# Kernel optimization log

Hardware: AMD Instinct MI355X
Metric: run time of the kernel (lower is better)

Reference implementation:

```python
import jax, jax.numpy as jnp
import numpy as np
import math

D = 2048
NH = 16
HD = D // NH
MULT = 4
EPS = 1e-6


def rmsnorm(x, g):
    norm = jax.lax.rsqrt(jnp.mean(x * x, axis=-1, keepdims=True) + EPS)
    return g * x * norm


def setup_inputs() -> dict:
    key = jax.random.key(0)
    ks = jax.random.split(key, 8)
    s = 0.02  # keep activations in a sane range
    return {
        "x": jax.random.normal(ks[0], (2, 2048, D), dtype=jnp.float32),
        "g1": jnp.ones((D,), dtype=jnp.float32),
        "wq": jax.random.normal(ks[1], (D, D), dtype=jnp.float32) * s,
        "wk": jax.random.normal(ks[2], (D, D), dtype=jnp.float32) * s,
        "wv": jax.random.normal(ks[3], (D, D), dtype=jnp.float32) * s,
        "wo": jax.random.normal(ks[4], (D, D), dtype=jnp.float32) * s,
        "g2": jnp.ones((D,), dtype=jnp.float32),
        "w_up": jax.random.normal(ks[5], (2 * D * MULT, D), dtype=jnp.float32) * s,
        "w_down": jax.random.normal(ks[6], (D, D * MULT), dtype=jnp.float32) * s,
    }


def reference(x, g1, wq, wk, wv, wo, g2, w_up, w_down):
    B, T, _ = x.shape
    # --- causal self-attention with pre-RMSNorm ---
    h = rmsnorm(x, g1)
    q = (h @ wq.T).reshape(B, T, NH, HD).transpose(0, 2, 1, 3)  # [B,H,T,hd]
    k = (h @ wk.T).reshape(B, T, NH, HD).transpose(0, 2, 1, 3)
    v = (h @ wv.T).reshape(B, T, NH, HD).transpose(0, 2, 1, 3)
    att = jnp.einsum("bhtd,bhsd->bhts", q, k) / math.sqrt(HD)  # [B,H,T,T]
    neg = jnp.finfo(att.dtype).min
    causal = jnp.triu(jnp.full((T, T), neg, dtype=att.dtype), k=1)
    att = att + causal
    w = jax.nn.softmax(att, axis=-1)
    z = jnp.einsum("bhts,bhsd->bhtd", w, v)  # [B,H,T,hd]
    z = z.transpose(0, 2, 1, 3).reshape(B, T, D)
    x = x + z @ wo.T
    # --- SwiGLU-style FFN (GELU gate) with pre-RMSNorm ---
    h2 = rmsnorm(x, g2)
    uv = h2 @ w_up.T  # [B,T,2*D*MULT]
    u, vgate = jnp.split(uv, 2, axis=-1)
    ff = (jax.nn.gelu(u, approximate=False) * vgate) @ w_down.T
    return x + ff
```

## Files before the change

kernel.cpp:

```cpp
#include <hip/hip_runtime.h>
#include <math.h>

typedef __bf16 bf16_t;
typedef __bf16 bf16x8 __attribute__((ext_vector_type(8)));
typedef __bf16 bf16x4 __attribute__((ext_vector_type(4)));
typedef float f32x4 __attribute__((ext_vector_type(4)));

#define D_MODEL 2048
#define N_HEADS 16
#define HEAD_D 128
#define SEQ 2048
#define NTOK 4096
#define DFF 8192
#define UPN 16384

#define GLDS16(g, l) __builtin_amdgcn_global_load_lds( \
    (const __attribute__((address_space(1))) void*)(g), \
    (__attribute__((address_space(3))) void*)(l), 16, 0, 0)

#define MFMA16(a, b, c) __builtin_amdgcn_mfma_f32_16x16x32_bf16((a), (b), (c), 0, 0, 0)

__global__ __launch_bounds__(256) void cvt_bf16_kernel(const float* __restrict__ in,
                                                       bf16_t* __restrict__ out, long n4) {
    long i = (long)blockIdx.x * 256 + threadIdx.x;
    long stride = (long)gridDim.x * 256;
    for (; i < n4; i += stride) {
        float4 f = ((const float4*)in)[i];
        bf16x4 v;
        v[0] = (bf16_t)f.x; v[1] = (bf16_t)f.y; v[2] = (bf16_t)f.z; v[3] = (bf16_t)f.w;
        ((bf16x4*)out)[i] = v;
    }
}

__global__ __launch_bounds__(256) void rmsnorm_kernel(const float* __restrict__ x,
                                                      const float* __restrict__ g,
                                                      bf16_t* __restrict__ out) {
    int row = blockIdx.x;
    const float* xr = x + (size_t)row * D_MODEL;
    int c0 = threadIdx.x * 8;
    float4 a = *(const float4*)&xr[c0];
    float4 b = *(const float4*)&xr[c0 + 4];
    float ss = a.x*a.x + a.y*a.y + a.z*a.z + a.w*a.w
             + b.x*b.x + b.y*b.y + b.z*b.z + b.w*b.w;
    #pragma unroll
    for (int off = 1; off < 64; off <<= 1) ss += __shfl_xor(ss, off);
    __shared__ float red[4];
    if ((threadIdx.x & 63) == 0) red[threadIdx.x >> 6] = ss;
    __syncthreads();
    float norm = rsqrtf((red[0] + red[1] + red[2] + red[3]) * (1.f / D_MODEL) + 1e-6f);
    float4 ga = *(const float4*)&g[c0];
    float4 gb = *(const float4*)&g[c0 + 4];
    bf16x8 o;
    o[0] = (bf16_t)(a.x * ga.x * norm); o[1] = (bf16_t)(a.y * ga.y * norm);
    o[2] = (bf16_t)(a.z * ga.z * norm); o[3] = (bf16_t)(a.w * ga.w * norm);
    o[4] = (bf16_t)(b.x * gb.x * norm); o[5] = (bf16_t)(b.y * gb.y * norm);
    o[6] = (bf16_t)(b.z * gb.z * norm); o[7] = (bf16_t)(b.w * gb.w * norm);
    *(bf16x8*)&out[(size_t)row * D_MODEL + c0] = o;
}

__global__ __launch_bounds__(256) void combine3_kernel(const float* __restrict__ r,
        const float* __restrict__ p0, const float* __restrict__ p1,
        float* __restrict__ out, long n4) {
    long i = (long)blockIdx.x * 256 + threadIdx.x;
    long stride = (long)gridDim.x * 256;
    for (; i < n4; i += stride) {
        float4 a = ((const float4*)r)[i];
        float4 b = ((const float4*)p0)[i];
        float4 c = ((const float4*)p1)[i];
        float4 o; o.x = a.x+b.x+c.x; o.y = a.y+b.y+c.y; o.z = a.z+b.z+c.z; o.w = a.w+b.w+c.w;
        ((float4*)out)[i] = o;
    }
}

template<int MODE, int KSPLIT>
__global__ __launch_bounds__(512, 2)
void gemm256(const bf16_t* __restrict__ A, const bf16_t* __restrict__ W,
             void* __restrict__ o0, void* __restrict__ o1, void* __restrict__ o2,
             const float* __restrict__ res, int nbx, int K)
{
    __shared__ __align__(16) bf16_t ldsA[2 * 2 * 8192];
    __shared__ __align__(16) bf16_t ldsB[2 * 2 * 8192];
    const int tid = threadIdx.x;
    const int wave = tid >> 6, lane = tid & 63;
    const int lr = lane & 15, lg = lane >> 4;
    const int wm = wave >> 2, wn = wave & 3;

    const int nwg = gridDim.x, bid = blockIdx.x;
    const int cpx = nwg >> 3;
    const int s = (bid & 7) * cpx + (bid >> 3);
    const int by = s & 15, bx = s >> 4;
    const int bm0 = by * 256;
    const int bn0 = (MODE == 2) ? bx * 128 : bx * 256;
    const int z = (KSPLIT == 2) ? blockIdx.z : 0;
    const int Keff = K / KSPLIT, koff = z * Keff;

    const int rl = wave * 16 + (lane >> 2);
    const int gsw = ((lane & 3) ^ ((rl >> 1) & 3)) * 8;
    const bf16_t* asrc = A + (size_t)(bm0 + rl) * K + koff + gsw;
    const bf16_t* bsrc;
    size_t bstep2;
    if constexpr (MODE == 2) {
        int grp = rl >> 6, wi = rl & 63;
        int brow = (wi < 32) ? (bn0 + grp * 32 + wi) : (DFF + bn0 + grp * 32 + (wi - 32));
        bsrc = W + (size_t)brow * K + koff + gsw;
        bstep2 = (size_t)64 * K;
    } else {
        bsrc = W + (size_t)(bn0 + rl) * K + koff + gsw;
        bstep2 = (size_t)128 * K;
    }

    auto stA = [&](int t, int kh) {
        char* d = (char*)ldsA + (((t & 1) * 2 + kh) * 16384) + wave * 1024 + lane * 16;
        const bf16_t* sp = asrc + (size_t)t * 64 + kh * 32;
        GLDS16(sp, d);
        GLDS16(sp + (size_t)128 * K, d + 8192);
    };
    auto stB = [&](int t, int kh) {
        char* d = (char*)ldsB + (((t & 1) * 2 + kh) * 16384) + wave * 1024 + lane * 16;
        const bf16_t* sp = bsrc + (size_t)t * 64 + kh * 32;
        GLDS16(sp, d);
        GLDS16(sp + bstep2, d + 8192);
    };

    f32x4 acc[8][4] = {};
    const int xg = (lg ^ ((lr >> 1) & 3)) * 8;
    const int NKT = Keff >> 6;

    stA(0, 0); stA(0, 1); stB(0, 0); stB(0, 1); stA(1, 0);
    asm volatile("s_waitcnt vmcnt(2)" ::: "memory");
    __builtin_amdgcn_s_barrier();
    __builtin_amdgcn_sched_barrier(0);

    for (int t = 0; t < NKT; ++t) {
        const bf16_t* Ab = ldsA + ((t & 1) * 2) * 8192;
        const bf16_t* Bb = ldsB + ((t & 1) * 2) * 8192;
        const bool s1 = (t + 1 < NKT), s2 = (t + 2 < NKT);
        bf16x8 af[4], bfr[4];

        #pragma unroll
        for (int i = 0; i < 4; ++i)
            af[i] = *(const bf16x8*)&Ab[(wm * 128 + i * 16 + lr) * 32 + xg];
        #pragma unroll
        for (int n = 0; n < 4; ++n)
            bfr[n] = *(const bf16x8*)&Bb[(wn * 64 + n * 16 + lr) * 32 + xg];
        if (s1) { stA(t + 1, 1); stB(t + 1, 0); }
        __builtin_amdgcn_s_barrier();
        __builtin_amdgcn_sched_barrier(0);
        __builtin_amdgcn_s_setprio(1);
        #pragma unroll
        for (int i = 0; i < 4; ++i)
            #pragma unroll
            for (int n = 0; n < 4; ++n)
                acc[i][n] = MFMA16(af[i], bfr[n], acc[i][n]);
        __builtin_amdgcn_s_setprio(0);
        __builtin_amdgcn_s_barrier();
        __builtin_amdgcn_sched_barrier(0);

        #pragma unroll
        for (int i = 0; i < 4; ++i)
            af[i] = *(const bf16x8*)&Ab[(wm * 128 + (i + 4) * 16 + lr) * 32 + xg];
        if (s1) stB(t + 1, 1);
        __builtin_amdgcn_s_barrier();
        __builtin_amdgcn_sched_barrier(0);
        __builtin_amdgcn_s_setprio(1);
        #pragma unroll
        for (int i = 0; i < 4; ++i)
            #pragma unroll
            for (int n = 0; n < 4; ++n)
                acc[i + 4][n] = MFMA16(af[i], bfr[n], acc[i + 4][n]);
        __builtin_amdgcn_s_setprio(0);
        __builtin_amdgcn_s_barrier();
        __builtin_amdgcn_sched_barrier(0);

        #pragma unroll
        for (int i = 0; i < 4; ++i)
            af[i] = *(const bf16x8*)&Ab[8192 + (wm * 128 + i * 16 + lr) * 32 + xg];
        #pragma unroll
        for (int n = 0; n < 4; ++n)
            bfr[n] = *(const bf16x8*)&Bb[8192 + (wn * 64 + n * 16 + lr) * 32 + xg];
        __builtin_amdgcn_s_barrier();
        __builtin_amdgcn_sched_barrier(0);
        __builtin_amdgcn_s_setprio(1);
        #pragma unroll
        for (int i = 0; i < 4; ++i)
            #pragma unroll
            for (int n = 0; n < 4; ++n)
                acc[i][n] = MFMA16(af[i], bfr[n], acc[i][n]);
        __builtin_amdgcn_s_setprio(0);
        __builtin_amdgcn_s_barrier();
        __builtin_amdgcn_sched_barrier(0);

        #pragma unroll
        for (int i = 0; i < 4; ++i)
            af[i] = *(const bf16x8*)&Ab[8192 + (wm * 128 + (i + 4) * 16 + lr) * 32 + xg];
        if (s2) {
            stA(t + 2, 0);
            asm volatile("s_waitcnt vmcnt(2)" ::: "memory");
        } else {
            asm volatile("s_waitcnt vmcnt(0)" ::: "memory");
        }
        __builtin_amdgcn_s_barrier();
        __builtin_amdgcn_sched_barrier(0);
        __builtin_amdgcn_s_setprio(1);
        #pragma unroll
        for (int i = 0; i < 4; ++i)
            #pragma unroll
            for (int n = 0; n < 4; ++n)
                acc[i + 4][n] = MFMA16(af[i], bfr[n], acc[i + 4][n]);
        __builtin_amdgcn_s_setprio(0);
        __builtin_amdgcn_s_barrier();
        __builtin_amdgcn_sched_barrier(0);
    }

    if constexpr (MODE == 0) {
        const float qs = 0.08838834764831845f;
        const int th = bn0 >> 11;
        #pragma unroll
        for (int m = 0; m < 8; ++m) {
            int grow = bm0 + wm * 128 + m * 16 + lg * 4;
            #pragma unroll
            for (int n = 0; n < 4; ++n) {
                int gcol = bn0 + wn * 64 + n * 16 + lr;
                int c = gcol & 2047;
                if (th == 0) {
                    #pragma unroll
                    for (int r = 0; r < 4; ++r)
                        ((bf16_t*)o0)[(size_t)(grow + r) * D_MODEL + c] = (bf16_t)(acc[m][n][r] * qs);
                } else if (th == 1) {
                    #pragma unroll
                    for (int r = 0; r < 4; ++r)
                        ((bf16_t*)o1)[(size_t)(grow + r) * D_MODEL + c] = (bf16_t)acc[m][n][r];
                } else {
                    int hh = c >> 7, d = c & 127;
                    int bb = grow >> 11, t0 = grow & 2047;
                    bf16x4 st;
                    #pragma unroll
                    for (int r = 0; r < 4; ++r) st[r] = (bf16_t)acc[m][n][r];
                    *(bf16x4*)&((bf16_t*)o2)[((size_t)(bb * N_HEADS + hh) * HEAD_D + d) * SEQ + t0] = st;
                }
            }
        }
    } else if constexpr (MODE == 1) {
        float* po = (KSPLIT == 2) ? ((float*)o0 + (size_t)z * NTOK * D_MODEL) : (float*)o0;
        #pragma unroll
        for (int m = 0; m < 8; ++m) {
            int grow = bm0 + wm * 128 + m * 16 + lg * 4;
            #pragma unroll
            for (int n = 0; n < 4; ++n) {
                int gcol = bn0 + wn * 64 + n * 16 + lr;
                #pragma unroll
                for (int r = 0; r < 4; ++r) {
                    size_t idx = (size_t)(grow + r) * D_MODEL + gcol;
                    if (KSPLIT == 2) po[idx] = acc[m][n][r];
                    else             po[idx] = res[idx] + acc[m][n][r];
                }
            }
        }
    } else {
        #pragma unroll
        for (int m = 0; m < 8; ++m) {
            int grow = bm0 + wm * 128 + m * 16 + lg * 4;
            #pragma unroll
            for (int n = 0; n < 2; ++n) {
                int gcol = bn0 + wn * 32 + n * 16 + lr;
                #pragma unroll
                for (int r = 0; r < 4; ++r) {
                    float u = acc[m][n][r], vg = acc[m][n + 2][r];
                    float ge = 0.5f * u * (1.f + erff(u * 0.70710678118654752f));
                    ((bf16_t*)o0)[(size_t)(grow + r) * DFF + gcol] = (bf16_t)(ge * vg);
                }
            }
        }
    }
}

__global__ __launch_bounds__(256)
void attn_kernel(const bf16_t* __restrict__ Q, const bf16_t* __restrict__ K,
                 const bf16_t* __restrict__ Vt, bf16_t* __restrict__ Z)
{
    const int qt = gridDim.x - 1 - blockIdx.x;
    const int h = blockIdx.y, b = blockIdx.z;
    const int q0 = qt * 64;
    const int tid = threadIdx.x, wave = tid >> 6, lane = tid & 63;
    const int lr = lane & 15, lg = lane >> 4;

    __shared__ __align__(16) bf16_t Qs[64 * 136];
    __shared__ __align__(16) bf16_t Ks[64 * 136];
    __shared__ __align__(16) bf16_t Vts[128 * 72];
    __shared__ __align__(16) bf16_t Ps[4][16 * 72];

    const size_t base = ((size_t)b * SEQ) * D_MODEL + (size_t)h * HEAD_D;
    const size_t vbase = (size_t)(b * N_HEADS + h) * HEAD_D * SEQ;

    #pragma unroll
    for (int i = 0; i < 4; ++i) {
        int v = tid + 256 * i;
        int row = v >> 4, cv = (v & 15) * 8;
        *(uint4*)&Qs[row * 136 + cv] = *(const uint4*)&Q[base + (size_t)(q0 + row) * D_MODEL + cv];
    }

    f32x4 o[8] = {};
    float mrun[4], lrun[4];
    #pragma unroll
    for (int r = 0; r < 4; ++r) { mrun[r] = -1e30f; lrun[r] = 0.f; }

    for (int kt = 0; kt <= qt; ++kt) {
        const int k0 = kt * 64;
        __syncthreads();
        #pragma unroll
        for (int i = 0; i < 4; ++i) {
            int v = tid + 256 * i;
            int row = v >> 4, cv = (v & 15) * 8;
            *(uint4*)&Ks[row * 136 + cv] = *(const uint4*)&K[base + (size_t)(k0 + row) * D_MODEL + cv];
            int d = v >> 3, c8 = (v & 7) * 8;
            *(uint4*)&Vts[d * 72 + c8] = *(const uint4*)&Vt[vbase + (size_t)d * SEQ + k0 + c8];
        }
        __syncthreads();

        f32x4 sv[4] = {};
        #pragma unroll
        for (int kk = 0; kk < 4; ++kk) {
            bf16x8 aq = *(const bf16x8*)&Qs[(wave * 16 + lr) * 136 + kk * 32 + lg * 8];
            #pragma unroll
            for (int nb = 0; nb < 4; ++nb) {
                bf16x8 bk = *(const bf16x8*)&Ks[(nb * 16 + lr) * 136 + kk * 32 + lg * 8];
                sv[nb] = MFMA16(aq, bk, sv[nb]);
            }
        }
        if (kt == qt) {
            #pragma unroll
            for (int nb = 0; nb < 4; ++nb)
                #pragma unroll
                for (int r = 0; r < 4; ++r) {
                    int qrel = 16 * wave + lg * 4 + r;
                    int krel = nb * 16 + lr;
                    if (krel > qrel) sv[nb][r] = -1e30f;
                }
        }
        float resc[4];
        #pragma unroll
        for (int r = 0; r < 4; ++r) {
            float mx = fmaxf(fmaxf(sv[0][r], sv[1][r]), fmaxf(sv[2][r], sv[3][r]));
            #pragma unroll
            for (int off = 1; off < 16; off <<= 1) mx = fmaxf(mx, __shfl_xor(mx, off));
            float mnew = fmaxf(mrun[r], mx);
            resc[r] = __expf(mrun[r] - mnew);
            float sum = 0.f;
            #pragma unroll
            for (int nb = 0; nb < 4; ++nb) {
                float p = __expf(sv[nb][r] - mnew);
                sv[nb][r] = p;
                sum += p;
            }
            #pragma unroll
            for (int off = 1; off < 16; off <<= 1) sum += __shfl_xor(sum, off);
            lrun[r] = lrun[r] * resc[r] + sum;
            mrun[r] = mnew;
        }
        #pragma unroll
        for (int ob = 0; ob < 8; ++ob)
            #pragma unroll
            for (int r = 0; r < 4; ++r) o[ob][r] *= resc[r];
        #pragma unroll
        for (int nb = 0; nb < 4; ++nb)
            #pragma unroll
            for (int r = 0; r < 4; ++r)
                Ps[wave][(lg * 4 + r) * 72 + nb * 16 + lr] = (bf16_t)sv[nb][r];
        #pragma unroll
        for (int kk = 0; kk < 2; ++kk) {
            bf16x8 ap = *(const bf16x8*)&Ps[wave][lr * 72 + kk * 32 + lg * 8];
            #pragma unroll
            for (int ob = 0; ob < 8; ++ob) {
                bf16x8 bv = *(const bf16x8*)&Vts[(ob * 16 + lr) * 72 + kk * 32 + lg * 8];
                o[ob] = MFMA16(ap, bv, o[ob]);
            }
        }
    }
    #pragma unroll
    for (int ob = 0; ob < 8; ++ob)
        #pragma unroll
        for (int r = 0; r < 4; ++r) {
            int t = q0 + 16 * wave + lg * 4 + r;
            Z[base + (size_t)t * D_MODEL + ob * 16 + lr] = (bf16_t)(o[ob][r] / lrun[r]);
        }
}

extern "C" void kernel_launch(void* const* d_in, const int* in_sizes, int n_in,
                              void* d_out, int out_size, void* d_ws, size_t ws_size,
                              hipStream_t stream)
{
    const float* x   = (const float*)d_in[0];
    const float* g1  = (const float*)d_in[1];
    const float* wq  = (const float*)d_in[2];
    const float* wk  = (const float*)d_in[3];
    const float* wv  = (const float*)d_in[4];
    const float* wo  = (const float*)d_in[5];
    const float* g2  = (const float*)d_in[6];
    const float* wup = (const float*)d_in[7];
    const float* wdn = (const float*)d_in[8];
    float* out = (float*)d_out;

    char* wsp = (char*)d_ws;
    size_t off = 0;
    auto alloc = [&](size_t bytes) { void* p = wsp + off; off += (bytes + 255) & ~255ull; return p; };
    bf16_t* wq_b  = (bf16_t*)alloc((size_t)D_MODEL * D_MODEL * 2);
    bf16_t* wk_b  = (bf16_t*)alloc((size_t)D_MODEL * D_MODEL * 2);
    bf16_t* wv_b  = (bf16_t*)alloc((size_t)D_MODEL * D_MODEL * 2);
    bf16_t* wo_b  = (bf16_t*)alloc((size_t)D_MODEL * D_MODEL * 2);
    bf16_t* wup_b = (bf16_t*)alloc((size_t)UPN * D_MODEL * 2);
    bf16_t* wdn_b = (bf16_t*)alloc((size_t)D_MODEL * DFF * 2);
    bf16_t* h_b   = (bf16_t*)alloc((size_t)NTOK * D_MODEL * 2);
    bf16_t* q_b   = (bf16_t*)alloc((size_t)NTOK * D_MODEL * 2);
    bf16_t* k_b   = (bf16_t*)alloc((size_t)NTOK * D_MODEL * 2);
    bf16_t* vt_b  = (bf16_t*)alloc((size_t)NTOK * D_MODEL * 2);
    bf16_t* z_b   = (bf16_t*)alloc((size_t)NTOK * D_MODEL * 2);
    float*  x1    = (float*) alloc((size_t)NTOK * D_MODEL * 4);
    bf16_t* h2_b  = (bf16_t*)alloc((size_t)NTOK * D_MODEL * 2);
    bf16_t* act_b = (bf16_t*)alloc((size_t)NTOK * DFF * 2);
    float* pbuf = (float*)h_b;

    auto cvt = [&](const float* in, bf16_t* outb, long n) {
        long n4 = n / 4;
        long nb = (n4 + 255) / 256;
        int blocks = nb > 2048 ? 2048 : (int)nb;
        cvt_bf16_kernel<<<blocks, 256, 0, stream>>>(in, outb, n4);
    };
    cvt(wq,  wq_b,  (long)D_MODEL * D_MODEL);
    cvt(wk,  wk_b,  (long)D_MODEL * D_MODEL);
    cvt(wv,  wv_b,  (long)D_MODEL * D_MODEL);
    cvt(wo,  wo_b,  (long)D_MODEL * D_MODEL);
    cvt(wup, wup_b, (long)UPN * D_MODEL);
    cvt(wdn, wdn_b, (long)D_MODEL * DFF);

    rmsnorm_kernel<<<NTOK, 256, 0, stream>>>(x, g1, h_b);

    gemm256<0, 1><<<24 * 16, 512, 0, stream>>>(h_b, wq_b, q_b, k_b, vt_b, nullptr, 24, D_MODEL);

    attn_kernel<<<dim3(SEQ / 64, N_HEADS, 2), 256, 0, stream>>>(q_b, k_b, vt_b, z_b);

    gemm256<1, 2><<<dim3(8 * 16, 1, 2), 512, 0, stream>>>(z_b, wo_b, pbuf, nullptr, nullptr, nullptr, 8, D_MODEL);
    combine3_kernel<<<2048, 256, 0, stream>>>(x, pbuf, pbuf + (size_t)NTOK * D_MODEL, x1,
                                              (long)NTOK * D_MODEL / 4);

    rmsnorm_kernel<<<NTOK, 256, 0, stream>>>(x1, g2, h2_b);

    gemm256<2, 1><<<64 * 16, 512, 0, stream>>>(h2_b, wup_b, act_b, nullptr, nullptr, nullptr, 64, D_MODEL);

    gemm256<1, 2><<<dim3(8 * 16, 1, 2), 512, 0, stream>>>(act_b, wdn_b, pbuf, nullptr, nullptr, nullptr, 8, DFF);
    combine3_kernel<<<2048, 256, 0, stream>>>(x1, pbuf, pbuf + (size_t)NTOK * D_MODEL, out,
                                              (long)NTOK * D_MODEL / 4);
}
```

Before: 1.054 ms.

## Cut GEMM main-loop barriers from eight to two per k-tile

Restructures the bf16 GEMM inner loop so each 64-wide k-tile uses two workgroup barriers instead of eight. The per-quarter barriers and sched_barriers between LDS fragment loads and MFMA groups are gone, and B fragments now sit in separate registers (b0/b1). The aim is to cut barrier stalls and let the compiler interleave LDS reads with MFMAs across waves. In exchange it uses more VGPRs, and LDS reuse safety now rests on the single mid-tile barrier ordering the reads before the async prefetch into the same buffer.

```diff
diff --git a/kernel.cpp b/kernel.cpp
--- a/kernel.cpp
+++ b/kernel.cpp
@@ -129,87 +129,69 @@
     stA(0, 0); stA(0, 1); stB(0, 0); stB(0, 1); stA(1, 0);
     asm volatile("s_waitcnt vmcnt(2)" ::: "memory");
     __builtin_amdgcn_s_barrier();
-    __builtin_amdgcn_sched_barrier(0);
 
     for (int t = 0; t < NKT; ++t) {
         const bf16_t* Ab = ldsA + ((t & 1) * 2) * 8192;
         const bf16_t* Bb = ldsB + ((t & 1) * 2) * 8192;
         const bool s1 = (t + 1 < NKT), s2 = (t + 2 < NKT);
-        bf16x8 af[4], bfr[4];
-
-        #pragma unroll
-        for (int i = 0; i < 4; ++i)
-            af[i] = *(const bf16x8*)&Ab[(wm * 128 + i * 16 + lr) * 32 + xg];
+        bf16x8 a0[4], a1[4], b0[4], b1[4];
+
+        #pragma unroll
+        for (int i = 0; i < 4; ++i)
+            a0[i] = *(const bf16x8*)&Ab[(wm * 128 + i * 16 + lr) * 32 + xg];
         #pragma unroll
         for (int n = 0; n < 4; ++n)
-            bfr[n] = *(const bf16x8*)&Bb[(wn * 64 + n * 16 + lr) * 32 + xg];
+            b0[n] = *(const bf16x8*)&Bb[(wn * 64 + n * 16 + lr) * 32 + xg];
         if (s1) { stA(t + 1, 1); stB(t + 1, 0); }
-        __builtin_amdgcn_s_barrier();
-        __builtin_amdgcn_sched_barrier(0);
         __builtin_amdgcn_s_setprio(1);
         #pragma unroll
         for (int i = 0; i < 4; ++i)
             #pragma unroll
             for (int n = 0; n < 4; ++n)
-                acc[i][n] = MFMA16(af[i], bfr[n], acc[i][n]);
+                acc[i][n] = MFMA16(a0[i], b0[n], acc[i][n]);
+        __builtin_amdgcn_s_setprio(0);
+
+        #pragma unroll
+        for (int i = 0; i < 4; ++i)
+            a1[i] = *(const bf16x8*)&Ab[(wm * 128 + (i + 4) * 16 + lr) * 32 + xg];
+        if (s1) stB(t + 1, 1);
+        __builtin_amdgcn_s_setprio(1);
+        #pragma unroll
+        for (int i = 0; i < 4; ++i)
+            #pragma unroll
+            for (int n = 0; n < 4; ++n)
+                acc[i + 4][n] = MFMA16(a1[i], b0[n], acc[i + 4][n]);
         __builtin_amdgcn_s_setprio(0);
         __builtin_amdgcn_s_barrier();
-        __builtin_amdgcn_sched_barrier(0);
-
-        #pragma unroll
-        for (int i = 0; i < 4; ++i)
-            af[i] = *(const bf16x8*)&Ab[(wm * 128 + (i + 4) * 16 + lr) * 32 + xg];
-        if (s1) stB(t + 1, 1);
+
+        #pragma unroll
+        for (int i = 0; i < 4; ++i)
+            a0[i] = *(const bf16x8*)&Ab[8192 + (wm * 128 + i * 16 + lr) * 32 + xg];
+        #pragma unroll
+        for (int n = 0; n < 4; ++n)
+            b1[n] = *(const bf16x8*)&Bb[8192 + (wn * 64 + n * 16 + lr) * 32 + xg];
+        __builtin_amdgcn_s_setprio(1);
+        #pragma unroll
+        for (int i = 0; i < 4; ++i)
+            #pragma unroll
+            for (int n = 0; n < 4; ++n)
+                acc[i][n] = MFMA16(a0[i], b1[n], acc[i][n]);
+        __builtin_amdgcn_s_setprio(0);
+
+        #pragma unroll
+        for (int i = 0; i < 4; ++i)
+            a1[i] = *(const bf16x8*)&Ab[8192 + (wm * 128 + (i + 4) * 16 + lr) * 32 + xg];
+        if (s2) stA(t + 2, 0);
+        __builtin_amdgcn_s_setprio(1);
+        #pragma unroll
+        for (int i = 0; i < 4; ++i)
+            #pragma unroll
+            for (int n = 0; n < 4; ++n)
+                acc[i + 4][n] = MFMA16(a1[i], b1[n], acc[i + 4][n]);
+        __builtin_amdgcn_s_setprio(0);
+        if (s2) asm volatile("s_waitcnt vmcnt(2)" ::: "memory");
+        else    asm volatile("s_waitcnt vmcnt(0)" ::: "memory");
         __builtin_amdgcn_s_barrier();
-        __builtin_amdgcn_sched_barrier(0);
-        __builtin_amdgcn_s_setprio(1);
-        #pragma unroll
-        for (int i = 0; i < 4; ++i)
-            #pragma unroll
-            for (int n = 0; n < 4; ++n)
-                acc[i + 4][n] = MFMA16(af[i], bfr[n], acc[i + 4][n]);
-        __builtin_amdgcn_s_setprio(0);
-        __builtin_amdgcn_s_barrier();
-        __builtin_amdgcn_sched_barrier(0);
-
-        #pragma unroll
-        for (int i = 0; i < 4; ++i)
-            af[i] = *(const bf16x8*)&Ab[8192 + (wm * 128 + i * 16 + lr) * 32 + xg];
-        #pragma unroll
-        for (int n = 0; n < 4; ++n)
-            bfr[n] = *(const bf16x8*)&Bb[8192 + (wn * 64 + n * 16 + lr) * 32 + xg];
-        __builtin_amdgcn_s_barrier();
-        __builtin_amdgcn_sched_barrier(0);
-        __builtin_amdgcn_s_setprio(1);
-        #pragma unroll
-        for (int i = 0; i < 4; ++i)
-            #pragma unroll
-            for (int n = 0; n < 4; ++n)
-                acc[i][n] = MFMA16(af[i], bfr[n], acc[i][n]);
-        __builtin_amdgcn_s_setprio(0);
-        __builtin_amdgcn_s_barrier();
-        __builtin_amdgcn_sched_barrier(0);
-
-        #pragma unroll
-        for (int i = 0; i < 4; ++i)
-            af[i] = *(const bf16x8*)&Ab[8192 + (wm * 128 + (i + 4) * 16 + lr) * 32 + xg];
-        if (s2) {
-            stA(t + 2, 0);
-            asm volatile("s_waitcnt vmcnt(2)" ::: "memory");
-        } else {
-            asm volatile("s_waitcnt vmcnt(0)" ::: "memory");
-        }
-        __builtin_amdgcn_s_barrier();
-        __builtin_amdgcn_sched_barrier(0);
-        __builtin_amdgcn_s_setprio(1);
-        #pragma unroll
-        for (int i = 0; i < 4; ++i)
-            #pragma unroll
-            for (int n = 0; n < 4; ++n)
-                acc[i + 4][n] = MFMA16(af[i], bfr[n], acc[i + 4][n]);
-        __builtin_amdgcn_s_setprio(0);
-        __builtin_amdgcn_s_barrier();
-        __builtin_amdgcn_sched_barrier(0);
     }
 
     if constexpr (MODE == 0) {
```

Result: faster. 1.006 ms (-4.6%).
